# Kernel optimization log

Measured on AMD Instinct MI355X. Metric: run time of the kernel, lower is better.

The kernel has to match this reference:

```python
import jax, jax.numpy as jnp
import numpy as np
from jax import lax

EPS = 1e-5  # torch BatchNorm2d default


def setup_inputs() -> dict:
    key = jax.random.key(0)
    k1, k2 = jax.random.split(key)
    x = jax.random.normal(k1, (8, 32, 28, 28), dtype=jnp.float32)
    # AdderConv.param: [out_channel, in_channel, k, k], init ~ N(0,1)
    W = jax.random.normal(k2, (64, 32, 3, 3), dtype=jnp.float32)
    # BatchNorm2d affine params at init
    gamma = jnp.ones((64,), dtype=jnp.float32)
    beta = jnp.zeros((64,), dtype=jnp.float32)
    return {"x": x, "W": W, "gamma": gamma, "beta": beta}


def _adder(patches, Wc):
    # patches: [N, K, Ho, Wo] with K = C*kh*kw (channel-major, matching torch unfold)
    # Wc: [O, K]
    # AdderNet: out[n,o,ho,wo] = -sum_k |patches[n,k,ho,wo] - Wc[o,k]|
    diff = patches[:, None, :, :, :] - Wc[None, :, :, None, None]  # [N,O,K,Ho,Wo]
    return -jnp.abs(diff).sum(axis=2)  # [N,O,Ho,Wo]


def reference(x, W, gamma, beta):
    O, C, kh, kw = W.shape
    # im2col, same layout as torch.nn.functional.unfold: feature dim = C*kh*kw
    patches = lax.conv_general_dilated_patches(
        x, (kh, kw), window_strides=(1, 1), padding=[(1, 1), (1, 1)]
    )  # [N, C*kh*kw, Ho, Wo]
    Wc = W.reshape(O, C * kh * kw)
    out = _adder(patches, Wc)  # [N, O, Ho, Wo]
    # BatchNorm2d, training mode (batch statistics, biased variance)
    mean = out.mean(axis=(0, 2, 3), keepdims=True)
    var = out.var(axis=(0, 2, 3), keepdims=True)
    y = (out - mean) * lax.rsqrt(var + EPS)
    return y * gamma[None, :, None, None] + beta[None, :, None, None]
```

## Files before the change

### kernel.cpp

```cpp
#include <hip/hip_runtime.h>

#define NB   8
#define CIN  32
#define HH   28
#define WW   28
#define OC   64
#define HWSZ (HH*WW)
#define TOTAL (NB*OC*HWSZ)
#define CNT  (NB*HWSZ)

#define KSPLIT 4
#define KH     (CIN/KSPLIT)
#define TROWS  6
#define TCOLS  30
#define TSZ    (KH*TROWS*TCOLS)

#define CPW    4

__global__ __launch_bounds__(256) void adder_kernel(
    const float* __restrict__ x, const float* __restrict__ Wt,
    float* __restrict__ rawp)
{
    __shared__ float xs[TSZ];
    const int t     = threadIdx.x;
    const int bid   = blockIdx.x;
    const int ks    = bid & 3;
    const int chgrp = (bid >> 2) & 3;
    const int rq    = (bid >> 4) % 7;
    const int n     = bid / (16 * 7);
    const int h0    = rq * 4;
    const int c0    = ks * KH;

    for (int i = t; i < TSZ; i += 256) {
        int cc  = i / (TROWS*TCOLS);
        int rem = i % (TROWS*TCOLS);
        int r   = rem / TCOLS;
        int col = rem % TCOLS;
        int hh  = h0 - 1 + r;
        int ww  = col - 1;
        float v = 0.0f;
        if (hh >= 0 && hh < HH && ww >= 0 && ww < WW)
            v = x[((n*CIN + (c0+cc))*HH + hh)*WW + ww];
        xs[i] = v;
    }
    __syncthreads();

    const int lane = t & 63;
    const int g    = __builtin_amdgcn_readfirstlane(t >> 6);
    const int rg   = lane >> 5;
    const int pl   = lane & 31;
    const bool valid = pl < WW;
    const int pw   = valid ? pl : 0;
    const int o_base = chgrp*16 + g*CPW;

    float acc[2][CPW];
    #pragma unroll
    for (int pix = 0; pix < 2; ++pix)
        #pragma unroll
        for (int oo = 0; oo < CPW; ++oo) acc[pix][oo] = 0.0f;

    #pragma unroll
    for (int cc = 0; cc < KH; ++cc) {
        float xr[4][3];
        const int b0 = (cc*TROWS + 2*rg)*TCOLS + pw;
        #pragma unroll
        for (int dr = 0; dr < 4; ++dr)
            #pragma unroll
            for (int dc = 0; dc < 3; ++dc)
                xr[dr][dc] = xs[b0 + dr*TCOLS + dc];

        #pragma unroll
        for (int oo = 0; oo < CPW; ++oo) {
            const float* wp = Wt + ((o_base + oo)*CIN + (c0 + cc))*9;
            #pragma unroll
            for (int dr = 0; dr < 3; ++dr)
                #pragma unroll
                for (int dc = 0; dc < 3; ++dc) {
                    float w = wp[dr*3+dc];
                    acc[0][oo] += __builtin_fabsf(xr[dr][dc]   - w);
                    acc[1][oo] += __builtin_fabsf(xr[dr+1][dc] - w);
                }
        }
    }

    if (valid) {
        float* rawh = rawp + ks * TOTAL;
        #pragma unroll
        for (int pix = 0; pix < 2; ++pix) {
            const int hh = h0 + 2*rg + pix;
            #pragma unroll
            for (int oo = 0; oo < CPW; ++oo)
                rawh[((n*OC + o_base + oo)*HH + hh)*WW + pw] = -acc[pix][oo];
        }
    }
}

__global__ __launch_bounds__(256) void stats_kernel(
    const float* __restrict__ rawp,
    const float* __restrict__ gamma, const float* __restrict__ beta,
    float* __restrict__ sc)
{
    const int o = blockIdx.x;
    const int t = threadIdx.x;
    const float4* r0 = (const float4*)rawp;
    const float4* r1 = (const float4*)(rawp + TOTAL);
    const float4* r2 = (const float4*)(rawp + 2*TOTAL);
    const float4* r3 = (const float4*)(rawp + 3*TOTAL);
    double s = 0.0, s2 = 0.0;
    for (int i4 = t; i4 < CNT/4; i4 += 256) {
        int nn  = i4 / (HWSZ/4);
        int pos = i4 % (HWSZ/4);
        int idx = (nn*OC + o)*(HWSZ/4) + pos;
        float4 a = r0[idx], b = r1[idx], c = r2[idx], d = r3[idx];
        float vx = (a.x + b.x) + (c.x + d.x);
        float vy = (a.y + b.y) + (c.y + d.y);
        float vz = (a.z + b.z) + (c.z + d.z);
        float vw = (a.w + b.w) + (c.w + d.w);
        s  += (double)vx + (double)vy + (double)vz + (double)vw;
        s2 += (double)vx*vx + (double)vy*vy + (double)vz*vz + (double)vw*vw;
    }
    #pragma unroll
    for (int off = 32; off >= 1; off >>= 1) {
        s  += __shfl_xor(s,  off, 64);
        s2 += __shfl_xor(s2, off, 64);
    }
    __shared__ double ls[4], ls2[4];
    const int lane = t & 63, w = t >> 6;
    if (lane == 0) { ls[w] = s; ls2[w] = s2; }
    __syncthreads();
    if (t == 0) {
        double S  = ls[0] + ls[1] + ls[2] + ls[3];
        double S2 = ls2[0] + ls2[1] + ls2[2] + ls2[3];
        double mean = S * (1.0 / CNT);
        double var  = S2 * (1.0 / CNT) - mean * mean;
        double inv  = 1.0 / sqrt(var + 1e-5);
        double scl  = (double)gamma[o] * inv;
        sc[o]       = (float)scl;
        sc[64 + o]  = (float)((double)beta[o] - mean * scl);
    }
}

__global__ __launch_bounds__(256) void bn_kernel(
    const float* __restrict__ rawp, const float* __restrict__ sc,
    float* __restrict__ out)
{
    int i4 = blockIdx.x * 256 + threadIdx.x;
    if (i4 >= TOTAL/4) return;
    int o = (i4 / (HWSZ/4)) & (OC - 1);
    float s = sc[o];
    float b = sc[64 + o];
    float4 a0 = ((const float4*)rawp)[i4];
    float4 a1 = ((const float4*)(rawp + TOTAL))[i4];
    float4 a2 = ((const float4*)(rawp + 2*TOTAL))[i4];
    float4 a3 = ((const float4*)(rawp + 3*TOTAL))[i4];
    float4 v;
    v.x = ((a0.x + a1.x) + (a2.x + a3.x)) * s + b;
    v.y = ((a0.y + a1.y) + (a2.y + a3.y)) * s + b;
    v.z = ((a0.z + a1.z) + (a2.z + a3.z)) * s + b;
    v.w = ((a0.w + a1.w) + (a2.w + a3.w)) * s + b;
    ((float4*)out)[i4] = v;
}

extern "C" void kernel_launch(void* const* d_in, const int* in_sizes, int n_in,
                              void* d_out, int out_size, void* d_ws, size_t ws_size,
                              hipStream_t stream) {
    const float* x     = (const float*)d_in[0];
    const float* Wt    = (const float*)d_in[1];
    const float* gamma = (const float*)d_in[2];
    const float* beta  = (const float*)d_in[3];
    float* out = (float*)d_out;

    float* sc   = (float*)d_ws;
    float* rawp = (float*)((char*)d_ws + 4096);

    adder_kernel<<<NB*7*4*KSPLIT, 256, 0, stream>>>(x, Wt, rawp);
    stats_kernel<<<OC, 256, 0, stream>>>(rawp, gamma, beta, sc);
    bn_kernel<<<(TOTAL/4 + 255) / 256, 256, 0, stream>>>(rawp, sc, out);
}
```

Baseline: 80.26 us.

## Split input channels eight ways and preload all input windows into registers

Doubles the channel split from 4 to 8 partial sums, which doubles the adder grid to 1792 blocks. It also loads all per-channel input windows from LDS into registers up front and reorders the loops to iterate output channels outermost. It adds a min-blocks hint to launch_bounds. The aim is more parallelism and occupancy in the adder stage. In exchange, the stats and BN kernels must read and sum twice as many partial buffers, which adds global memory traffic and needs a larger workspace.

```diff
diff --git a/kernel.cpp b/kernel.cpp
--- a/kernel.cpp
+++ b/kernel.cpp
@@ -9,7 +9,7 @@
 #define TOTAL (NB*OC*HWSZ)
 #define CNT  (NB*HWSZ)
 
-#define KSPLIT 4
+#define KSPLIT 8
 #define KH     (CIN/KSPLIT)
 #define TROWS  6
 #define TCOLS  30
@@ -17,17 +17,17 @@
 
 #define CPW    4
 
-__global__ __launch_bounds__(256) void adder_kernel(
+__global__ __launch_bounds__(256, 4) void adder_kernel(
     const float* __restrict__ x, const float* __restrict__ Wt,
     float* __restrict__ rawp)
 {
     __shared__ float xs[TSZ];
     const int t     = threadIdx.x;
     const int bid   = blockIdx.x;
-    const int ks    = bid & 3;
-    const int chgrp = (bid >> 2) & 3;
-    const int rq    = (bid >> 4) % 7;
-    const int n     = bid / (16 * 7);
+    const int ks    = bid & 7;
+    const int chgrp = (bid >> 3) & 3;
+    const int rq    = (bid >> 5) % 7;
+    const int n     = bid / (32 * 7);
     const int h0    = rq * 4;
     const int c0    = ks * KH;
 
@@ -53,6 +53,17 @@
     const int pw   = valid ? pl : 0;
     const int o_base = chgrp*16 + g*CPW;
 
+    float xr[KH][4][3];
+    #pragma unroll
+    for (int cc = 0; cc < KH; ++cc) {
+        const int b0 = (cc*TROWS + 2*rg)*TCOLS + pw;
+        #pragma unroll
+        for (int dr = 0; dr < 4; ++dr)
+            #pragma unroll
+            for (int dc = 0; dc < 3; ++dc)
+                xr[cc][dr][dc] = xs[b0 + dr*TCOLS + dc];
+    }
+
     float acc[2][CPW];
     #pragma unroll
     for (int pix = 0; pix < 2; ++pix)
@@ -60,25 +71,17 @@
         for (int oo = 0; oo < CPW; ++oo) acc[pix][oo] = 0.0f;
 
     #pragma unroll
-    for (int cc = 0; cc < KH; ++cc) {
-        float xr[4][3];
-        const int b0 = (cc*TROWS + 2*rg)*TCOLS + pw;
+    for (int oo = 0; oo < CPW; ++oo) {
+        const float* wp = Wt + ((o_base + oo)*CIN + c0)*9;
         #pragma unroll
-        for (int dr = 0; dr < 4; ++dr)
-            #pragma unroll
-            for (int dc = 0; dc < 3; ++dc)
-                xr[dr][dc] = xs[b0 + dr*TCOLS + dc];
-
-        #pragma unroll
-        for (int oo = 0; oo < CPW; ++oo) {
-            const float* wp = Wt + ((o_base + oo)*CIN + (c0 + cc))*9;
+        for (int cc = 0; cc < KH; ++cc) {
             #pragma unroll
             for (int dr = 0; dr < 3; ++dr)
                 #pragma unroll
                 for (int dc = 0; dc < 3; ++dc) {
-                    float w = wp[dr*3+dc];
-                    acc[0][oo] += __builtin_fabsf(xr[dr][dc]   - w);
-                    acc[1][oo] += __builtin_fabsf(xr[dr+1][dc] - w);
+                    float w = wp[cc*9 + dr*3 + dc];
+                    acc[0][oo] += __builtin_fabsf(xr[cc][dr][dc]   - w);
+                    acc[1][oo] += __builtin_fabsf(xr[cc][dr+1][dc] - w);
                 }
         }
     }
@@ -102,22 +105,19 @@
 {
     const int o = blockIdx.x;
     const int t = threadIdx.x;
-    const float4* r0 = (const float4*)rawp;
-    const float4* r1 = (const float4*)(rawp + TOTAL);
-    const float4* r2 = (const float4*)(rawp + 2*TOTAL);
-    const float4* r3 = (const float4*)(rawp + 3*TOTAL);
     double s = 0.0, s2 = 0.0;
     for (int i4 = t; i4 < CNT/4; i4 += 256) {
         int nn  = i4 / (HWSZ/4);
         int pos = i4 % (HWSZ/4);
         int idx = (nn*OC + o)*(HWSZ/4) + pos;
-        float4 a = r0[idx], b = r1[idx], c = r2[idx], d = r3[idx];
-        float vx = (a.x + b.x) + (c.x + d.x);
-        float vy = (a.y + b.y) + (c.y + d.y);
-        float vz = (a.z + b.z) + (c.z + d.z);
-        float vw = (a.w + b.w) + (c.w + d.w);
-        s  += (double)vx + (double)vy + (double)vz + (double)vw;
-        s2 += (double)vx*vx + (double)vy*vy + (double)vz*vz + (double)vw*vw;
+        float4 a = ((const float4*)rawp)[idx];
+        #pragma unroll
+        for (int k = 1; k < KSPLIT; ++k) {
+            float4 b = ((const float4*)(rawp + (size_t)k*TOTAL))[idx];
+            a.x += b.x; a.y += b.y; a.z += b.z; a.w += b.w;
+        }
+        s  += (double)a.x + (double)a.y + (double)a.z + (double)a.w;
+        s2 += (double)a.x*a.x + (double)a.y*a.y + (double)a.z*a.z + (double)a.w*a.w;
     }
     #pragma unroll
     for (int off = 32; off >= 1; off >>= 1) {
@@ -149,15 +149,17 @@
     int o = (i4 / (HWSZ/4)) & (OC - 1);
     float s = sc[o];
     float b = sc[64 + o];
-    float4 a0 = ((const float4*)rawp)[i4];
-    float4 a1 = ((const float4*)(rawp + TOTAL))[i4];
-    float4 a2 = ((const float4*)(rawp + 2*TOTAL))[i4];
-    float4 a3 = ((const float4*)(rawp + 3*TOTAL))[i4];
+    float4 a = ((const float4*)rawp)[i4];
+    #pragma unroll
+    for (int k = 1; k < KSPLIT; ++k) {
+        float4 c = ((const float4*)(rawp + (size_t)k*TOTAL))[i4];
+        a.x += c.x; a.y += c.y; a.z += c.z; a.w += c.w;
+    }
     float4 v;
-    v.x = ((a0.x + a1.x) + (a2.x + a3.x)) * s + b;
-    v.y = ((a0.y + a1.y) + (a2.y + a3.y)) * s + b;
-    v.z = ((a0.z + a1.z) + (a2.z + a3.z)) * s + b;
-    v.w = ((a0.w + a1.w) + (a2.w + a3.w)) * s + b;
+    v.x = a.x * s + b;
+    v.y = a.y * s + b;
+    v.z = a.z * s + b;
+    v.w = a.w * s + b;
     ((float4*)out)[i4] = v;
 }
 
```

New measurement: 82.28 us. 2.5% more time.

## Drop K-split, fuse BN statistics into adder kernel via double atomics

Applied to the files above, without the earlier changes.

Removes the 4-way input-channel split, so each block accumulates all 32 channels and writes one raw output buffer instead of four partial buffers. Per-channel sum and sum-of-squares are now reduced with wave shuffles inside the adder kernel and added to a zeroed stats array with double atomics, which removes the separate stats kernel. The BN kernel recomputes scale and shift per thread and reads a single buffer. In exchange the grid shrinks from 896 to 224 blocks, cutting parallelism for the main compute kernel, and the shared tile grows fourfold.

```diff
diff --git a/kernel.cpp b/kernel.cpp
--- a/kernel.cpp
+++ b/kernel.cpp
@@ -9,27 +9,23 @@
 #define TOTAL (NB*OC*HWSZ)
 #define CNT  (NB*HWSZ)
 
-#define KSPLIT 4
-#define KH     (CIN/KSPLIT)
-#define TROWS  6
-#define TCOLS  30
-#define TSZ    (KH*TROWS*TCOLS)
+#define TROWS 6
+#define TCOLS 30
+#define TSZ   (CIN*TROWS*TCOLS)
 
-#define CPW    4
+#define CPW   4
 
 __global__ __launch_bounds__(256) void adder_kernel(
     const float* __restrict__ x, const float* __restrict__ Wt,
-    float* __restrict__ rawp)
+    float* __restrict__ raw, double* __restrict__ stats)
 {
     __shared__ float xs[TSZ];
     const int t     = threadIdx.x;
     const int bid   = blockIdx.x;
-    const int ks    = bid & 3;
-    const int chgrp = (bid >> 2) & 3;
-    const int rq    = (bid >> 4) % 7;
-    const int n     = bid / (16 * 7);
+    const int chgrp = bid & 3;
+    const int rq    = (bid >> 2) % 7;
+    const int n     = bid / 28;
     const int h0    = rq * 4;
-    const int c0    = ks * KH;
 
     for (int i = t; i < TSZ; i += 256) {
         int cc  = i / (TROWS*TCOLS);
@@ -40,7 +36,7 @@
         int ww  = col - 1;
         float v = 0.0f;
         if (hh >= 0 && hh < HH && ww >= 0 && ww < WW)
-            v = x[((n*CIN + (c0+cc))*HH + hh)*WW + ww];
+            v = x[((n*CIN + cc)*HH + hh)*WW + ww];
         xs[i] = v;
     }
     __syncthreads();
@@ -59,8 +55,8 @@
         #pragma unroll
         for (int oo = 0; oo < CPW; ++oo) acc[pix][oo] = 0.0f;
 
-    #pragma unroll
-    for (int cc = 0; cc < KH; ++cc) {
+    #pragma unroll 4
+    for (int cc = 0; cc < CIN; ++cc) {
         float xr[4][3];
         const int b0 = (cc*TROWS + 2*rg)*TCOLS + pw;
         #pragma unroll
@@ -71,7 +67,7 @@
 
         #pragma unroll
         for (int oo = 0; oo < CPW; ++oo) {
-            const float* wp = Wt + ((o_base + oo)*CIN + (c0 + cc))*9;
+            const float* wp = Wt + ((o_base + oo)*CIN + cc)*9;
             #pragma unroll
             for (int dr = 0; dr < 3; ++dr)
                 #pragma unroll
@@ -84,80 +80,53 @@
     }
 
     if (valid) {
-        float* rawh = rawp + ks * TOTAL;
         #pragma unroll
         for (int pix = 0; pix < 2; ++pix) {
             const int hh = h0 + 2*rg + pix;
             #pragma unroll
             for (int oo = 0; oo < CPW; ++oo)
-                rawh[((n*OC + o_base + oo)*HH + hh)*WW + pw] = -acc[pix][oo];
+                raw[((n*OC + o_base + oo)*HH + hh)*WW + pw] = -acc[pix][oo];
+        }
+    }
+
+    #pragma unroll
+    for (int oo = 0; oo < CPW; ++oo) {
+        float v0 = valid ? -acc[0][oo] : 0.0f;
+        float v1 = valid ? -acc[1][oo] : 0.0f;
+        float s  = v0 + v1;
+        float s2 = v0*v0 + v1*v1;
+        #pragma unroll
+        for (int off = 32; off >= 1; off >>= 1) {
+            s  += __shfl_xor(s,  off, 64);
+            s2 += __shfl_xor(s2, off, 64);
+        }
+        if (lane == 0) {
+            atomicAdd(&stats[o_base + oo],      (double)s);
+            atomicAdd(&stats[64 + o_base + oo], (double)s2);
         }
     }
 }
 
-__global__ __launch_bounds__(256) void stats_kernel(
-    const float* __restrict__ rawp,
+__global__ __launch_bounds__(256) void bn_kernel(
+    const float* __restrict__ raw, const double* __restrict__ stats,
     const float* __restrict__ gamma, const float* __restrict__ beta,
-    float* __restrict__ sc)
-{
-    const int o = blockIdx.x;
-    const int t = threadIdx.x;
-    const float4* r0 = (const float4*)rawp;
-    const float4* r1 = (const float4*)(rawp + TOTAL);
-    const float4* r2 = (const float4*)(rawp + 2*TOTAL);
-    const float4* r3 = (const float4*)(rawp + 3*TOTAL);
-    double s = 0.0, s2 = 0.0;
-    for (int i4 = t; i4 < CNT/4; i4 += 256) {
-        int nn  = i4 / (HWSZ/4);
-        int pos = i4 % (HWSZ/4);
-        int idx = (nn*OC + o)*(HWSZ/4) + pos;
-        float4 a = r0[idx], b = r1[idx], c = r2[idx], d = r3[idx];
-        float vx = (a.x + b.x) + (c.x + d.x);
-        float vy = (a.y + b.y) + (c.y + d.y);
-        float vz = (a.z + b.z) + (c.z + d.z);
-        float vw = (a.w + b.w) + (c.w + d.w);
-        s  += (double)vx + (double)vy + (double)vz + (double)vw;
-        s2 += (double)vx*vx + (double)vy*vy + (double)vz*vz + (double)vw*vw;
-    }
-    #pragma unroll
-    for (int off = 32; off >= 1; off >>= 1) {
-        s  += __shfl_xor(s,  off, 64);
-        s2 += __shfl_xor(s2, off, 64);
-    }
-    __shared__ double ls[4], ls2[4];
-    const int lane = t & 63, w = t >> 6;
-    if (lane == 0) { ls[w] = s; ls2[w] = s2; }
-    __syncthreads();
-    if (t == 0) {
-        double S  = ls[0] + ls[1] + ls[2] + ls[3];
-        double S2 = ls2[0] + ls2[1] + ls2[2] + ls2[3];
-        double mean = S * (1.0 / CNT);
-        double var  = S2 * (1.0 / CNT) - mean * mean;
-        double inv  = 1.0 / sqrt(var + 1e-5);
-        double scl  = (double)gamma[o] * inv;
-        sc[o]       = (float)scl;
-        sc[64 + o]  = (float)((double)beta[o] - mean * scl);
-    }
-}
-
-__global__ __launch_bounds__(256) void bn_kernel(
-    const float* __restrict__ rawp, const float* __restrict__ sc,
     float* __restrict__ out)
 {
     int i4 = blockIdx.x * 256 + threadIdx.x;
     if (i4 >= TOTAL/4) return;
     int o = (i4 / (HWSZ/4)) & (OC - 1);
-    float s = sc[o];
-    float b = sc[64 + o];
-    float4 a0 = ((const float4*)rawp)[i4];
-    float4 a1 = ((const float4*)(rawp + TOTAL))[i4];
-    float4 a2 = ((const float4*)(rawp + 2*TOTAL))[i4];
-    float4 a3 = ((const float4*)(rawp + 3*TOTAL))[i4];
+    double mean = stats[o] * (1.0 / CNT);
+    double var  = stats[64 + o] * (1.0 / CNT) - mean * mean;
+    double inv  = 1.0 / sqrt(var + 1e-5);
+    double scl  = (double)gamma[o] * inv;
+    float s = (float)scl;
+    float b = (float)((double)beta[o] - mean * scl);
+    float4 a = ((const float4*)raw)[i4];
     float4 v;
-    v.x = ((a0.x + a1.x) + (a2.x + a3.x)) * s + b;
-    v.y = ((a0.y + a1.y) + (a2.y + a3.y)) * s + b;
-    v.z = ((a0.z + a1.z) + (a2.z + a3.z)) * s + b;
-    v.w = ((a0.w + a1.w) + (a2.w + a3.w)) * s + b;
+    v.x = a.x * s + b;
+    v.y = a.y * s + b;
+    v.z = a.z * s + b;
+    v.w = a.w * s + b;
     ((float4*)out)[i4] = v;
 }
 
@@ -170,10 +139,11 @@
     const float* beta  = (const float*)d_in[3];
     float* out = (float*)d_out;
 
-    float* sc   = (float*)d_ws;
-    float* rawp = (float*)((char*)d_ws + 4096);
+    double* stats = (double*)d_ws;
+    float*  raw   = (float*)((char*)d_ws + 4096);
 
-    adder_kernel<<<NB*7*4*KSPLIT, 256, 0, stream>>>(x, Wt, rawp);
-    stats_kernel<<<OC, 256, 0, stream>>>(rawp, gamma, beta, sc);
-    bn_kernel<<<(TOTAL/4 + 255) / 256, 256, 0, stream>>>(rawp, sc, out);
+    hipMemsetAsync(d_ws, 0, 1024, stream);
+
+    adder_kernel<<<NB*7*4, 256, 0, stream>>>(x, Wt, raw, stats);
+    bn_kernel<<<(TOTAL/4 + 255) / 256, 256, 0, stream>>>(raw, stats, gamma, beta, out);
 }
```

Measured after the change: 99.85 us. 24.4% more time.
